# Kernel tuning notes

Measured on AMD Instinct MI355X. Metric: run time of the kernel, lower is better.

## Reference

```python
import jax, jax.numpy as jnp
import numpy as np

K_REGION = 32
C_CONTEXT = 128
CONF_THR = 0.5


def safe_normalize(x):
    return x / jnp.maximum(x.sum(axis=-1, keepdims=True), 1e-6)


def _geometry(mask_grid, h, w):
    # mask_grid: [B, K, h*w] -> per-mask bbox (x_min,y_min,x_max,y_max) + area, vectorized
    B, K, _ = mask_grid.shape
    m2 = mask_grid.reshape(B, K, h, w)
    present = m2 > 0.05
    rows = present.any(-1)  # [B,K,h]
    cols = present.any(-2)  # [B,K,w]
    yi = jnp.arange(h)
    xi = jnp.arange(w)
    y_min = jnp.min(jnp.where(rows, yi, h), axis=-1).astype(jnp.float32)
    y_max = jnp.max(jnp.where(rows, yi, -1), axis=-1).astype(jnp.float32)
    x_min = jnp.min(jnp.where(cols, xi, w), axis=-1).astype(jnp.float32)
    x_max = jnp.max(jnp.where(cols, xi, -1), axis=-1).astype(jnp.float32)
    hden = float(max(h - 1, 1))
    wden = float(max(w - 1, 1))
    area = present.astype(jnp.float32).mean(axis=(-1, -2))
    geom = jnp.stack([x_min / wden, y_min / hden, x_max / wden, y_max / hden, area], axis=-1)
    has_any = present.any(axis=(-1, -2))
    return jnp.where(has_any[..., None], geom, 0.0).astype(mask_grid.dtype)


def setup_inputs():
    key = jax.random.key(0)
    ks = jax.random.split(key, 16)
    B, N, D, M, Hm, Wm, Qd, Hd = 8, 576, 1024, 64, 384, 384, 4096, 1024
    inp = {}
    inp['patch_tokens'] = jax.random.normal(ks[0], (B, N, D), jnp.float32)
    inp['masks'] = jax.random.uniform(ks[1], (B, M, Hm, Wm), jnp.float32)
    inp['scores'] = jax.random.uniform(ks[2], (B, M), jnp.float32)
    inp['question_embed'] = jax.random.normal(ks[3], (B, Qd), jnp.float32)
    s = 0.02
    inp['W1'] = jax.random.normal(ks[4], (5, D), jnp.float32) * s
    inp['b1'] = jnp.zeros((D,), jnp.float32)
    inp['W2'] = jax.random.normal(ks[5], (D, D), jnp.float32) * s
    inp['b2'] = jnp.zeros((D,), jnp.float32)
    inp['Wv'] = jax.random.normal(ks[6], (D, Hd), jnp.float32) * s
    inp['bv'] = jnp.zeros((Hd,), jnp.float32)
    inp['Wp'] = jax.random.normal(ks[7], (1, Hd), jnp.float32) * s
    inp['bp'] = jnp.zeros((Hd,), jnp.float32)
    inp['Wq'] = jax.random.normal(ks[8], (Qd, Hd), jnp.float32) * s
    inp['bq'] = jnp.zeros((Hd,), jnp.float32)
    inp['Wo'] = jax.random.normal(ks[9], (Hd, 1), jnp.float32) * s
    inp['bo'] = jnp.zeros((1,), jnp.float32)
    inp['type_emb'] = jax.random.normal(ks[10], (3, D), jnp.float32) * s
    inp['patch_h'] = 24
    inp['patch_w'] = 24
    return inp


def reference(patch_tokens, masks, scores, question_embed, W1, b1, W2, b2,
              Wv, bv, Wp, bp, Wq, bq, Wo, bo, type_emb, patch_h, patch_w):
    B, N, D = patch_tokens.shape
    h, w = patch_h, patch_w
    M = masks.shape[1]

    grounding_valid = (masks.reshape(B, M, -1).sum(-1) > 0).any(-1)  # [B]

    order = jnp.argsort(-scores, axis=1)
    scores_s = jnp.take_along_axis(scores, order, axis=1)
    masks_s = jnp.take_along_axis(masks, order[:, :, None, None], axis=1)
    masks_k = masks_s[:, :K_REGION]
    scores_k = scores_s[:, :K_REGION]
    valid = scores_k >= CONF_THR
    masks_k = masks_k * valid[:, :, None, None].astype(masks_k.dtype)
    scores_k = jnp.where(valid, scores_k, 0.0)

    # MaskDownsampler: adaptive avg pool (exact: Hm,Wm divisible by h,w)
    Hm, Wm = masks_k.shape[-2:]
    fh, fw = Hm // h, Wm // w
    mg = masks_k.reshape(B, K_REGION, h, fh, w, fw).mean(axis=(3, 5)).reshape(B, K_REGION, h * w)

    uniform = jnp.full((B, K_REGION, N), 1.0 / N, dtype=patch_tokens.dtype)
    mg = jnp.where(grounding_valid[:, None, None], mg, uniform)
    scores_k = jnp.where(grounding_valid[:, None], scores_k, 1.0)

    # RegionPooler
    nm = safe_normalize(jnp.maximum(mg, 0.0))
    pooled = jnp.einsum('bkn,bnd->bkd', nm, patch_tokens)
    weighted = pooled * scores_k[..., None]
    geom = _geometry(mg, h, w)  # [B,K,5]
    g = jax.nn.silu(geom @ W1 + b1) @ W2 + b2
    region_tokens = weighted + g

    patch_prior = (mg * scores_k[..., None]).sum(axis=1)
    patch_prior = safe_normalize(jnp.maximum(patch_prior, 0.0))
    patch_prior = jnp.where(grounding_valid[:, None], patch_prior, jnp.full_like(patch_prior, 1.0 / N))

    # RoutingScorer
    hid = jnp.tanh(patch_tokens @ Wv + bv
                   + patch_prior[:, :, None] @ Wp + bp
                   + (question_embed @ Wq + bq)[:, None, :])
    routing_scores = (hid @ Wo + bo)[..., 0]  # [B,N]
    routing_weights = jax.nn.softmax(routing_scores, axis=-1)

    top_k = min(C_CONTEXT, N)
    _, sel_idx = jax.lax.top_k(routing_scores, top_k)
    context_tokens = jnp.take_along_axis(patch_tokens, sel_idx[:, :, None], axis=1)
    sel_mask = jnp.zeros((B, N), patch_tokens.dtype).at[jnp.arange(B)[:, None], sel_idx].set(1.0)

    # BackgroundPooler
    residual = jnp.maximum(1.0 - sel_mask, 0.0)
    residual = residual / jnp.maximum(residual.sum(-1, keepdims=True), 1e-6)
    bg = jnp.einsum('bn,bnd->bd', residual, patch_tokens)

    region_tokens = region_tokens + type_emb[0][None, None, :]
    context_tokens = context_tokens + type_emb[1][None, None, :]
    background_token = bg[:, None, :] + type_emb[2][None, None, :]
    visual_tokens = jnp.concatenate([region_tokens, context_tokens, background_token], axis=1)

    return (visual_tokens, region_tokens, context_tokens, background_token,
            patch_prior, routing_weights, sel_idx, grounding_valid)
```

## Files before the change

### kernel.cpp

```cpp
#include <hip/hip_runtime.h>
#include <math.h>

typedef long long I64;

#define NB    8
#define NTOK  576
#define DIM   1024
#define NMASK 64
#define HMASK 384
#define WMASK 384
#define QDIM  4096
#define HDIM  1024
#define KREG  32
#define CCTX  128
#define GH    24
#define GW    24
#define GNUM  576

#define OFF_VIS 0
#define OFF_REG 1318912
#define OFF_CTX 1581056
#define OFF_BG  2629632
#define OFF_PP  2637824
#define OFF_RW  2642432
#define OFF_SEL 2647040
#define OFF_GV  2648064

#define WS_BS   0
#define WS_NMAT 294912
#define WS_SCK  442368
#define WS_H1   442624
#define WS_Q    704768
#define WS_Q2   712960
#define WS_GV   721152
#define WS_PP   721160
#define WS_CS   725768
#define WS_RS   733960
#define WS_RSP  738568
#define WS_HID  775432
#define WS_END  5494024

#define QBLK      256
#define BS_BLOCKS (NB * NMASK * 24)
#define MEGA_GRID (256 + 256 + BS_BLOCKS)

__global__ __launch_bounds__(256, 2) void k_mega(
    const float* __restrict__ masks, const float* __restrict__ qe,
    const float* __restrict__ Wq, const float* __restrict__ bq,
    const float* __restrict__ pt, const float* __restrict__ Wv,
    float* __restrict__ ws) {
  int gid = blockIdx.x;
  int t = threadIdx.x;
  __shared__ __align__(16) float smem[10432];

  if (gid < 256) {
    int b = gid >> 5;
    int r = gid & 31;
    int tokTile = r >> 3;
    int colTile = r & 7;
    int n0 = tokTile * 144;
    int col0 = colTile * 128;
    int trow = t >> 4;
    int tcol = t & 15;

    float (*sA)[36]  = (float(*)[36])smem;
    float (*sW)[164] = (float(*)[164])(smem + 5184);

    float acc[9][8];
    #pragma unroll
    for (int i = 0; i < 9; ++i)
      #pragma unroll
      for (int j = 0; j < 8; ++j) acc[i][j] = 0.f;

    int a_row0 = t >> 3, a_kq = t & 7;
    int a_row1 = (t + 256) >> 3;
    int a_row2 = (t + 512) >> 3;
    int a_row3 = (t + 768) >> 3;
    int a_row4 = (t + 1024) >> 3;
    int w_k0 = t >> 5, w_c = t & 31;

    const float* ptb = pt + (I64)(b * NTOK + n0) * DIM;
    const float* wvb = Wv + col0;

    float4 pa0, pa1, pa2, pa3, pa4 = {0,0,0,0};
    float4 pw0, pw1, pw2, pw3;

    pa0 = *(const float4*)&ptb[(I64)a_row0 * DIM + a_kq * 4];
    pa1 = *(const float4*)&ptb[(I64)a_row1 * DIM + a_kq * 4];
    pa2 = *(const float4*)&ptb[(I64)a_row2 * DIM + a_kq * 4];
    pa3 = *(const float4*)&ptb[(I64)a_row3 * DIM + a_kq * 4];
    if (t < 128) pa4 = *(const float4*)&ptb[(I64)a_row4 * DIM + a_kq * 4];
    pw0 = *(const float4*)&wvb[(I64)(w_k0 +  0) * HDIM + w_c * 4];
    pw1 = *(const float4*)&wvb[(I64)(w_k0 +  8) * HDIM + w_c * 4];
    pw2 = *(const float4*)&wvb[(I64)(w_k0 + 16) * HDIM + w_c * 4];
    pw3 = *(const float4*)&wvb[(I64)(w_k0 + 24) * HDIM + w_c * 4];

    for (int s = 0; s < 32; ++s) {
      __syncthreads();
      *(float4*)&sA[a_row0][a_kq * 4] = pa0;
      *(float4*)&sA[a_row1][a_kq * 4] = pa1;
      *(float4*)&sA[a_row2][a_kq * 4] = pa2;
      *(float4*)&sA[a_row3][a_kq * 4] = pa3;
      if (t < 128) *(float4*)&sA[a_row4][a_kq * 4] = pa4;
      *(float4*)&sW[w_k0 +  0][w_c * 4] = pw0;
      *(float4*)&sW[w_k0 +  8][w_c * 4] = pw1;
      *(float4*)&sW[w_k0 + 16][w_c * 4] = pw2;
      *(float4*)&sW[w_k0 + 24][w_c * 4] = pw3;
      __syncthreads();
      if (s + 1 < 32) {
        int k0 = (s + 1) * 32;
        pa0 = *(const float4*)&ptb[(I64)a_row0 * DIM + k0 + a_kq * 4];
        pa1 = *(const float4*)&ptb[(I64)a_row1 * DIM + k0 + a_kq * 4];
        pa2 = *(const float4*)&ptb[(I64)a_row2 * DIM + k0 + a_kq * 4];
        pa3 = *(const float4*)&ptb[(I64)a_row3 * DIM + k0 + a_kq * 4];
        if (t < 128) pa4 = *(const float4*)&ptb[(I64)a_row4 * DIM + k0 + a_kq * 4];
        pw0 = *(const float4*)&wvb[(I64)(k0 + w_k0 +  0) * HDIM + w_c * 4];
        pw1 = *(const float4*)&wvb[(I64)(k0 + w_k0 +  8) * HDIM + w_c * 4];
        pw2 = *(const float4*)&wvb[(I64)(k0 + w_k0 + 16) * HDIM + w_c * 4];
        pw3 = *(const float4*)&wvb[(I64)(k0 + w_k0 + 24) * HDIM + w_c * 4];
      }
      #pragma unroll 2
      for (int kk4 = 0; kk4 < 8; ++kk4) {
        float4 af[9];
        #pragma unroll
        for (int i = 0; i < 9; ++i)
          af[i] = *(const float4*)&sA[trow * 9 + i][kk4 * 4];
        float4 w0[4], w1[4];
        #pragma unroll
        for (int m = 0; m < 4; ++m) {
          w0[m] = *(const float4*)&sW[kk4 * 4 + m][tcol * 4];
          w1[m] = *(const float4*)&sW[kk4 * 4 + m][64 + tcol * 4];
        }
        #pragma unroll
        for (int i = 0; i < 9; ++i) {
          #pragma unroll
          for (int m = 0; m < 4; ++m) {
            float a = ((const float*)&af[i])[m];
            acc[i][0] = fmaf(a, w0[m].x, acc[i][0]);
            acc[i][1] = fmaf(a, w0[m].y, acc[i][1]);
            acc[i][2] = fmaf(a, w0[m].z, acc[i][2]);
            acc[i][3] = fmaf(a, w0[m].w, acc[i][3]);
            acc[i][4] = fmaf(a, w1[m].x, acc[i][4]);
            acc[i][5] = fmaf(a, w1[m].y, acc[i][5]);
            acc[i][6] = fmaf(a, w1[m].z, acc[i][6]);
            acc[i][7] = fmaf(a, w1[m].w, acc[i][7]);
          }
        }
      }
    }
    float* hid = ws + WS_HID + ((I64)b * NTOK + n0) * HDIM;
    #pragma unroll
    for (int i = 0; i < 9; ++i) {
      int row = trow * 9 + i;
      float4 va = {acc[i][0], acc[i][1], acc[i][2], acc[i][3]};
      float4 vb = {acc[i][4], acc[i][5], acc[i][6], acc[i][7]};
      *(float4*)&hid[(I64)row * HDIM + col0 + tcol * 4] = va;
      *(float4*)&hid[(I64)row * HDIM + col0 + 64 + tcol * 4] = vb;
    }
  } else if (gid < 512) {
    int g = gid - 256;
    int b = g >> 5, r = g & 31;
    int qb = r >> 1, ih = r & 1;
    int base = ih * 2048;
    float* qs = smem;
    float (*sp)[64] = (float(*)[64])(smem + 2048);
    const float4* s4 = (const float4*)(qe + (I64)b * QDIM + base);
    *(float4*)&qs[t * 4] = s4[t];
    *(float4*)&qs[(t + 256) * 4] = s4[t + 256];
    __syncthreads();
    int dl = t & 63, ig = t >> 6;
    int d = qb * 64 + dl;
    const float* wq = Wq + d;
    float a0 = 0.f, a1 = 0.f, a2 = 0.f, a3 = 0.f;
    float a4 = 0.f, a5 = 0.f, a6 = 0.f, a7 = 0.f;
    for (int i = ig; i < 2048; i += 32) {
      a0 = fmaf(qs[i],      wq[(I64)(base + i) * HDIM],      a0);
      a1 = fmaf(qs[i + 4],  wq[(I64)(base + i + 4) * HDIM],  a1);
      a2 = fmaf(qs[i + 8],  wq[(I64)(base + i + 8) * HDIM],  a2);
      a3 = fmaf(qs[i + 12], wq[(I64)(base + i + 12) * HDIM], a3);
      a4 = fmaf(qs[i + 16], wq[(I64)(base + i + 16) * HDIM], a4);
      a5 = fmaf(qs[i + 20], wq[(I64)(base + i + 20) * HDIM], a5);
      a6 = fmaf(qs[i + 24], wq[(I64)(base + i + 24) * HDIM], a6);
      a7 = fmaf(qs[i + 28], wq[(I64)(base + i + 28) * HDIM], a7);
    }
    sp[ig][dl] = ((a0 + a1) + (a2 + a3)) + ((a4 + a5) + (a6 + a7));
    __syncthreads();
    if (t < 64) {
      float s2 = (sp[0][t] + sp[1][t]) + (sp[2][t] + sp[3][t]);
      int dd = qb * 64 + t;
      ws[(ih ? WS_Q2 : WS_Q) + (I64)b * HDIM + dd] = s2 + (ih ? 0.f : bq[dd]);
    }
  } else {
    int g = gid - 512;
    int yband = g % 24;
    int bm = g / 24;
    float (*sm)[96] = (float(*)[96])smem;
    const float4* src = (const float4*)(masks + (I64)bm * (HMASK * WMASK) + (I64)yband * 16 * WMASK);
    #pragma unroll
    for (int j = 0; j < 6; ++j) {
      int f = t + 256 * j;
      float4 v = src[f];
      sm[f / 96][f % 96] = (v.x + v.y) + (v.z + v.w);
    }
    __syncthreads();
    if (t < 24) {
      float tt = 0.f;
      #pragma unroll
      for (int rr = 0; rr < 16; ++rr)
        #pragma unroll
        for (int c = 0; c < 4; ++c) tt += sm[rr][t * 4 + c];
      ws[WS_BS + (I64)bm * GNUM + yband * 24 + t] = tt;
    }
  }
}

__global__ __launch_bounds__(256) void k_epi(
    const float* __restrict__ bv, const float* __restrict__ bp,
    const float* __restrict__ Wp, const float* __restrict__ Wo,
    const float* __restrict__ bo, float* __restrict__ ws) {
  int t = threadIdx.x;
  int g = blockIdx.x * 16 + (t >> 4);
  int l = t & 15;
  int b = g / NTOK, n = g % NTOK;
  const float* hid = ws + WS_HID + (I64)g * HDIM;
  const float* q1 = ws + WS_Q + (I64)b * HDIM;
  const float* q2 = ws + WS_Q2 + (I64)b * HDIM;
  float ppv = ws[WS_PP + b * GNUM + n];
  float ssum = 0.f;
  #pragma unroll 4
  for (int j = 0; j < 16; ++j) {
    int c = l * 64 + j * 4;
    float4 h4 = *(const float4*)&hid[c];
    float4 b4 = *(const float4*)&bv[c];
    float4 p4 = *(const float4*)&bp[c];
    float4 w4 = *(const float4*)&Wp[c];
    float4 o4 = *(const float4*)&Wo[c];
    float4 qa = *(const float4*)&q1[c];
    float4 qb = *(const float4*)&q2[c];
    ssum = fmaf(o4.x, tanhf(h4.x + b4.x + p4.x + qa.x + qb.x + ppv * w4.x), ssum);
    ssum = fmaf(o4.y, tanhf(h4.y + b4.y + p4.y + qa.y + qb.y + ppv * w4.y), ssum);
    ssum = fmaf(o4.z, tanhf(h4.z + b4.z + p4.z + qa.z + qb.z + ppv * w4.z), ssum);
    ssum = fmaf(o4.w, tanhf(h4.w + b4.w + p4.w + qa.w + qb.w + ppv * w4.w), ssum);
  }
  ssum += __shfl_xor(ssum, 1);
  ssum += __shfl_xor(ssum, 2);
  ssum += __shfl_xor(ssum, 4);
  ssum += __shfl_xor(ssum, 8);
  if (l == 0) ws[WS_RS + g] = ssum + bo[0];
}

#define MGPAD 580
__global__ __launch_bounds__(256) void k_perbatch(
    const float* __restrict__ bs, const float* __restrict__ scores,
    const float* __restrict__ W1, const float* __restrict__ b1,
    float* __restrict__ ws, float* __restrict__ out) {
  int b = blockIdx.x;
  int t = threadIdx.x;
  __shared__ float s_mg[KREG][MGPAD];
  __shared__ float s_sc[NMASK];
  __shared__ float s_msum[NMASK];
  __shared__ int   s_order[NMASK];
  __shared__ float s_sck[KREG];
  __shared__ int   s_valid[KREG];
  __shared__ int   s_midx[KREG];
  __shared__ float s_rowsum[KREG];
  __shared__ float s_pp[GNUM];
  __shared__ float s_geom[KREG][5];
  __shared__ float s_red[64];
  __shared__ int   s_gv;
  __shared__ float s_ppsum;

  {
    int m = t >> 2, q = t & 3;
    const float4* p = (const float4*)(bs + ((I64)b * NMASK + m) * GNUM) + q * 36;
    float s = 0.f;
    #pragma unroll 4
    for (int j = 0; j < 36; ++j) {
      float4 v = p[j];
      s += v.x; s += v.y; s += v.z; s += v.w;
    }
    s += __shfl_xor(s, 1);
    s += __shfl_xor(s, 2);
    if (q == 0) s_msum[m] = s;
  }
  if (t < NMASK) s_sc[t] = scores[b * NMASK + t];
  __syncthreads();
  if (t == 0) {
    int g = 0;
    for (int m = 0; m < NMASK; ++m) g |= (s_msum[m] > 0.f) ? 1 : 0;
    s_gv = g;
  }
  if (t < NMASK) {
    float v = s_sc[t];
    int r = 0;
    for (int j = 0; j < NMASK; ++j) {
      float vj = s_sc[j];
      r += (vj > v) || (vj == v && j < t);
    }
    s_order[r] = t;
  }
  __syncthreads();
  const int gv = s_gv;
  if (t < KREG) {
    int m = s_order[t];
    float sc = s_sc[m];
    int valid = (sc >= 0.5f) ? 1 : 0;
    s_midx[t] = m;
    s_valid[t] = valid;
    float sck = gv ? (valid ? sc : 0.f) : 1.f;
    s_sck[t] = sck;
    ws[WS_SCK + b * KREG + t] = sck;
  }
  __syncthreads();
  {
    int k = t >> 3, sub = t & 7;
    const float inv256 = 1.f / 256.f;
    const float invN = 1.f / 576.f;
    float scale = gv ? (s_valid[k] ? inv256 : 0.f) : 0.f;
    float addv  = gv ? 0.f : invN;
    const float4* src = (const float4*)(bs + ((I64)b * NMASK + s_midx[k]) * GNUM) + sub * 18;
    float* dst = &s_mg[k][sub * 72];
    #pragma unroll 3
    for (int j = 0; j < 18; ++j) {
      float4 v = src[j];
      v.x = v.x * scale + addv;
      v.y = v.y * scale + addv;
      v.z = v.z * scale + addv;
      v.w = v.w * scale + addv;
      *(float4*)(dst + j * 4) = v;
    }
  }
// ... 14 lines not shown
    ws[WS_NMAT + ((I64)b * KREG + k) * GNUM + n] = v / fmaxf(s_rowsum[k], 1e-6f);
  }
  for (int n = t; n < GNUM; n += 256) {
    float raw = 0.f;
    #pragma unroll
    for (int k = 0; k < KREG; ++k) raw = fmaf(s_mg[k][n], s_sck[k], raw);
    s_pp[n] = fmaxf(raw, 0.f);
  }
  __syncthreads();
  if (t < 64) {
    float s = 0.f;
    for (int n = t; n < GNUM; n += 64) s += s_pp[n];
    s_red[t] = s;
  }
  __syncthreads();
  if (t == 0) {
    float s = 0.f;
    for (int i = 0; i < 64; ++i) s += s_red[i];
    s_ppsum = s;
  }
  __syncthreads();
  {
    const float invN = 1.f / 576.f;
    float den = fmaxf(s_ppsum, 1e-6f);
    for (int n = t; n < GNUM; n += 256) {
      float v = gv ? (s_pp[n] / den) : invN;
      ws[WS_PP + b * GNUM + n] = v;
      out[OFF_PP + b * GNUM + n] = v;
    }
  }
  {
    int k = t >> 3, sub = t & 7;
    unsigned colmask = 0u;
    int ymin = GH, ymax = -1, cnt = 0;
    #pragma unroll
    for (int yy = 0; yy < 3; ++yy) {
      int y = sub * 3 + yy;
      unsigned rowm = 0u;
      for (int x = 0; x < GW; ++x)
        if (s_mg[k][y * GW + x] > 0.05f) rowm |= (1u << x);
      if (rowm) { if (y < ymin) ymin = y; if (y > ymax) ymax = y; }
      colmask |= rowm;
      cnt += __popc(rowm);
    }
    #pragma unroll
    for (int off = 1; off < 8; off <<= 1) {
      colmask |= (unsigned)__shfl_xor((int)colmask, off);
      cnt += __shfl_xor(cnt, off);
      int o1 = __shfl_xor(ymin, off); ymin = (o1 < ymin) ? o1 : ymin;
      int o2 = __shfl_xor(ymax, off); ymax = (o2 > ymax) ? o2 : ymax;
    }
    if (sub == 0) {
      float g0, g1, g2, g3, g4;
      if (cnt > 0) {
        int xmin = __ffs(colmask) - 1;
        int xmax = 31 - __clz(colmask);
        g0 = (float)xmin / 23.f;
        g1 = (float)ymin / 23.f;
        g2 = (float)xmax / 23.f;
        g3 = (float)ymax / 23.f;
        g4 = (float)cnt / 576.f;
      } else { g0 = g1 = g2 = g3 = g4 = 0.f; }
      s_geom[k][0] = g0; s_geom[k][1] = g1; s_geom[k][2] = g2;
      s_geom[k][3] = g3; s_geom[k][4] = g4;
    }
  }
  __syncthreads();
  for (int idx = t; idx < KREG * HDIM; idx += 256) {
    int k = idx >> 10, j = idx & 1023;
    float x = 0.f;
    #pragma unroll
    for (int i = 0; i < 5; ++i) x += s_geom[k][i] * W1[i * HDIM + j];
    x += b1[j];
    float sg = 1.f / (1.f + expf(-x));
    ws[WS_H1 + ((I64)b * KREG + k) * HDIM + j] = x * sg;
  }
  if (t == 0) {
    float g = gv ? 1.f : 0.f;
    ws[WS_GV + b] = g;
    out[OFF_GV + b] = g;
  }
}

__global__ __launch_bounds__(512) void k_region(
    const float* __restrict__ pt, const float* __restrict__ W2,
    const float* __restrict__ b2, const float* __restrict__ te,
    float* __restrict__ ws, float* __restrict__ out) {
  int blk = blockIdx.x;
  int b = blk >> 6, kg = (blk >> 3) & 7, dg = blk & 7;
  int t = threadIdx.x;
  int dl = t & 127;
  int qh = t >> 7;
  int d = dg * 128 + dl;
  const float* nmb = ws + WS_NMAT + ((I64)b * KREG + kg * 4) * GNUM;
  const float* h1b = ws + WS_H1 + ((I64)b * KREG + kg * 4) * HDIM;
  float accP[4] = {0, 0, 0, 0};
  float accG[4] = {0, 0, 0, 0};
  float accS = 0.f;
  int n0 = qh * 144, n1 = n0 + 144;
  for (int n = n0; n < n1; ++n) {
    float p = pt[((I64)b * NTOK + n) * DIM + d];
    accS += p;
    #pragma unroll
    for (int kk = 0; kk < 4; ++kk)
      accP[kk] = fmaf(nmb[kk * GNUM + n], p, accP[kk]);
  }
  int j0 = qh * 256, j1 = j0 + 256;
  for (int j = j0; j < j1; ++j) {
    float wv = W2[(I64)j * DIM + d];
    #pragma unroll
    for (int kk = 0; kk < 4; ++kk)
      accG[kk] = fmaf(h1b[kk * HDIM + j], wv, accG[kk]);
  }
  __shared__ float cmbP[4][4][128];
  __shared__ float cmbG[4][4][128];
  __shared__ float cmbS[4][128];
  #pragma unroll
  for (int kk = 0; kk < 4; ++kk) {
    cmbP[qh][kk][dl] = accP[kk];
    cmbG[qh][kk][dl] = accG[kk];
  }
  cmbS[qh][dl] = accS;
  __syncthreads();
  if (qh == 0) {
    float bb = b2[d], t0 = te[d];
    #pragma unroll
    for (int kk = 0; kk < 4; ++kk) {
      int k = kg * 4 + kk;
      float P = (cmbP[0][kk][dl] + cmbP[1][kk][dl]) + (cmbP[2][kk][dl] + cmbP[3][kk][dl]);
      float G = (cmbG[0][kk][dl] + cmbG[1][kk][dl]) + (cmbG[2][kk][dl] + cmbG[3][kk][dl]);
      float val = P * ws[WS_SCK + b * KREG + k] + G + bb + t0;
      out[OFF_REG + ((I64)b * KREG + k) * DIM + d] = val;
      out[OFF_VIS + ((I64)b * 161 + k) * DIM + d] = val;
    }
    if (kg == 0)
      ws[WS_CS + (I64)b * DIM + d] =
          (cmbS[0][dl] + cmbS[1][dl]) + (cmbS[2][dl] + cmbS[3][dl]);
  }
}

__global__ __launch_bounds__(576) void k_soft2(float* __restrict__ ws, float* __restrict__ out) {
  int b = blockIdx.x, t = threadIdx.x;
  __shared__ float s_rs[NTOK];
  __shared__ float s_w[9];
  __shared__ float s_max, s_sum;
  s_rs[t] = ws[WS_RS + b * NTOK + t];
  __syncthreads();
  float v = s_rs[t];
  int r = 0;
  for (int j = 0; j < NTOK; ++j) {
    float vj = s_rs[j];
    r += (vj > v) || (vj == v && j < t);
  }
  float m = v;
  for (int off = 1; off < 64; off <<= 1) m = fmaxf(m, __shfl_xor(m, off));
  if ((t & 63) == 0) s_w[t >> 6] = m;
  __syncthreads();
  if (t == 0) {
    float mm = s_w[0];
    for (int i = 1; i < 9; ++i) mm = fmaxf(mm, s_w[i]);
    s_max = mm;
  }
  __syncthreads();
  float e = expf(v - s_max);
  float s = e;
  for (int off = 1; off < 64; off <<= 1) s += __shfl_xor(s, off);
  if ((t & 63) == 0) s_w[t >> 6] = s;
  __syncthreads();
  if (t == 0) {
    float ss = 0.f;
    for (int i = 0; i < 9; ++i) ss += s_w[i];
    s_sum = ss;
  }
  __syncthreads();
  out[OFF_RW + b * NTOK + t] = e / s_sum;
  if (r < CCTX) out[OFF_SEL + b * CCTX + r] = (float)t;
}

__global__ __launch_bounds__(256) void k_post(const float* __restrict__ pt, const float* __restrict__ te,
                                              const float* __restrict__ ws, const float* __restrict__ outr,
                                              float* __restrict__ out) {
  int rr = blockIdx.x, b = blockIdx.y;
  int d = threadIdx.x * 4;
  if (rr < CCTX) {
    int idx = (int)outr[OFF_SEL + b * CCTX + rr];
    float4 v = *(const float4*)&pt[((I64)b * NTOK + idx) * DIM + d];
    float4 e = *(const float4*)&te[DIM + d];
    v.x += e.x; v.y += e.y; v.z += e.z; v.w += e.w;
    *(float4*)&out[OFF_CTX + ((I64)b * CCTX + rr) * DIM + d] = v;
    *(float4*)&out[OFF_VIS + ((I64)b * 161 + KREG + rr) * DIM + d] = v;
  } else {
    float4 s = *(const float4*)&ws[WS_CS + (I64)b * DIM + d];
    for (int r = 0; r < CCTX; ++r) {
      int idx = (int)outr[OFF_SEL + b * CCTX + r];
      float4 v = *(const float4*)&pt[((I64)b * NTOK + idx) * DIM + d];
      s.x -= v.x; s.y -= v.y; s.z -= v.z; s.w -= v.w;
    }
    const float rinv = 1.f / 448.f;
    float4 e = *(const float4*)&te[2 * DIM + d];
    float4 o;
    o.x = s.x * rinv + e.x; o.y = s.y * rinv + e.y;
    o.z = s.z * rinv + e.z; o.w = s.w * rinv + e.w;
    *(float4*)&out[OFF_BG + (I64)b * DIM + d] = o;
    *(float4*)&out[OFF_VIS + ((I64)b * 161 + 160) * DIM + d] = o;
  }
}

__global__ __launch_bounds__(384) void k_bsq(const float* __restrict__ masks,
                                             const float* __restrict__ qe,
                                             const float* __restrict__ Wq,
                                             const float* __restrict__ bq,
                                             float* __restrict__ ws) {
  int gid = blockIdx.x;
  int t = threadIdx.x;
  __shared__ float shm[2048 + 6 * 64];
  if (gid >= QBLK) {
    int gid2 = gid - QBLK;
    int yband = gid2 % 24;
    int bm = gid2 / 24;
    float (*sm)[96] = (float(*)[96])shm;
    const float4* src = (const float4*)(masks + (I64)bm * (HMASK * WMASK) + (I64)yband * 16 * WMASK);
    float4 s4 = src[t];
    float4 v1 = src[t + 384];
    float4 v2 = src[t + 768];
    float4 v3 = src[t + 1152];
    s4.x += v1.x; s4.y += v1.y; s4.z += v1.z; s4.w += v1.w;
    s4.x += v2.x; s4.y += v2.y; s4.z += v2.z; s4.w += v2.w;
    s4.x += v3.x; s4.y += v3.y; s4.z += v3.z; s4.w += v3.w;
    float s = (s4.x + s4.y) + (s4.z + s4.w);
    sm[t / 96][t % 96] = s;
    __syncthreads();
    if (t < 24) {
      float tt = 0.f;
      #pragma unroll
      for (int rg = 0; rg < 4; ++rg)
        #pragma unroll
        for (int c = 0; c < 4; ++c) tt += sm[rg][t * 4 + c];
      ws[WS_BS + (I64)bm * GNUM + yband * 24 + t] = tt;
    }
  } else {
    int b = gid >> 5;
    int r = gid & 31;
    int qb = r >> 1;
    int ih = r & 1;
    int base = ih * 2048;
    float* qs = shm;
    float (*sp)[64] = (float(*)[64])(shm + 2048);
    {
      const float4* s4 = (const float4*)(qe + (I64)b * QDIM + base);
      float4 v = s4[t];
      *(float4*)&qs[t * 4] = v;
      if (t < 128) {
        float4 v2 = s4[t + 384];
        *(float4*)&qs[(t + 384) * 4] = v2;
      }
    }
    __syncthreads();
    int dl = t & 63, ig = t >> 6;
    int d = qb * 64 + dl;
    const float* wq = Wq + d;
    float a0 = 0.f, a1 = 0.f, a2 = 0.f, a3 = 0.f;
    float a4 = 0.f, a5 = 0.f, a6 = 0.f, a7 = 0.f;
    int i = ig;
    for (; i + 42 < 2048; i += 48) {
      a0 = fmaf(qs[i],      wq[(I64)(base + i) * HDIM],      a0);
      a1 = fmaf(qs[i + 6],  wq[(I64)(base + i + 6) * HDIM],  a1);
      a2 = fmaf(qs[i + 12], wq[(I64)(base + i + 12) * HDIM], a2);
      a3 = fmaf(qs[i + 18], wq[(I64)(base + i + 18) * HDIM], a3);
      a4 = fmaf(qs[i + 24], wq[(I64)(base + i + 24) * HDIM], a4);
      a5 = fmaf(qs[i + 30], wq[(I64)(base + i + 30) * HDIM], a5);
      a6 = fmaf(qs[i + 36], wq[(I64)(base + i + 36) * HDIM], a6);
      a7 = fmaf(qs[i + 42], wq[(I64)(base + i + 42) * HDIM], a7);
    }
    for (; i < 2048; i += 6)
      a0 = fmaf(qs[i], wq[(I64)(base + i) * HDIM], a0);
    sp[ig][dl] = ((a0 + a1) + (a2 + a3)) + ((a4 + a5) + (a6 + a7));
    __syncthreads();
    if (t < 64) {
      float s2 = ((sp[0][t] + sp[1][t]) + (sp[2][t] + sp[3][t])) + (sp[4][t] + sp[5][t]);
      int dd = qb * 64 + t;
      float outv = s2 + (ih ? 0.f : bq[dd]);
      ws[(ih ? WS_Q2 : WS_Q) + (I64)b * HDIM + dd] = outv;
    }
  }
}

__global__ __launch_bounds__(256, 1) void k_hid4(
// ... 76 lines not shown
      #pragma unroll
      for (int i = 0; i < 9; ++i)
        af[i] = *(const float4*)&sA[cur][trow * 9 + i][kk4 * 4];
      float4 w0[4], w1[4];
      #pragma unroll
      for (int m = 0; m < 4; ++m) {
        w0[m] = *(const float4*)&sW[cur][kk4 * 4 + m][tcol * 4];
        w1[m] = *(const float4*)&sW[cur][kk4 * 4 + m][64 + tcol * 4];
      }
      #pragma unroll
      for (int i = 0; i < 9; ++i) {
        #pragma unroll
        for (int m = 0; m < 4; ++m) {
          float a = ((const float*)&af[i])[m];
          acc[i][0] = fmaf(a, w0[m].x, acc[i][0]);
          acc[i][1] = fmaf(a, w0[m].y, acc[i][1]);
          acc[i][2] = fmaf(a, w0[m].z, acc[i][2]);
          acc[i][3] = fmaf(a, w0[m].w, acc[i][3]);
          acc[i][4] = fmaf(a, w1[m].x, acc[i][4]);
          acc[i][5] = fmaf(a, w1[m].y, acc[i][5]);
          acc[i][6] = fmaf(a, w1[m].z, acc[i][6]);
          acc[i][7] = fmaf(a, w1[m].w, acc[i][7]);
        }
      }
    }
    if (s + 1 < 32) {
      int nxt = (s + 1) & 1;
      *(float4*)&sA[nxt][a_row0][a_kq0 * 4] = pa0;
      *(float4*)&sA[nxt][a_row1][a_kq0 * 4] = pa1;
      *(float4*)&sA[nxt][a_row2][a_kq0 * 4] = pa2;
      *(float4*)&sA[nxt][a_row3][a_kq0 * 4] = pa3;
      if (t < 128) *(float4*)&sA[nxt][a_row4][a_kq0 * 4] = pa4;
      *(float4*)&sW[nxt][w_k0 +  0][w_c * 4] = pw0;
      *(float4*)&sW[nxt][w_k0 +  8][w_c * 4] = pw1;
      *(float4*)&sW[nxt][w_k0 + 16][w_c * 4] = pw2;
      *(float4*)&sW[nxt][w_k0 + 24][w_c * 4] = pw3;
    }
  }

  int ca = col0 + tcol * 4;
  int cb = col0 + 64 + tcol * 4;
  float4 bvA = *(const float4*)&bv[ca], bvB = *(const float4*)&bv[cb];
  float4 bpA = *(const float4*)&bp[ca], bpB = *(const float4*)&bp[cb];
  float4 wpA = *(const float4*)&Wp[ca], wpB = *(const float4*)&Wp[cb];
  float4 woA = *(const float4*)&Wo[ca], woB = *(const float4*)&Wo[cb];
  float4 qaA = *(const float4*)&ws[WS_Q  + (I64)b * HDIM + ca];
  float4 qaB = *(const float4*)&ws[WS_Q  + (I64)b * HDIM + cb];
  float4 qbA = *(const float4*)&ws[WS_Q2 + (I64)b * HDIM + ca];
  float4 qbB = *(const float4*)&ws[WS_Q2 + (I64)b * HDIM + cb];
  float bvv[8] = {bvA.x, bvA.y, bvA.z, bvA.w, bvB.x, bvB.y, bvB.z, bvB.w};
  float bpv[8] = {bpA.x, bpA.y, bpA.z, bpA.w, bpB.x, bpB.y, bpB.z, bpB.w};
  float wpv[8] = {wpA.x, wpA.y, wpA.z, wpA.w, wpB.x, wpB.y, wpB.z, wpB.w};
  float wov[8] = {woA.x, woA.y, woA.z, woA.w, woB.x, woB.y, woB.z, woB.w};
  float qv[8]  = {qaA.x + qbA.x, qaA.y + qbA.y, qaA.z + qbA.z, qaA.w + qbA.w,
                  qaB.x + qbB.x, qaB.y + qbB.y, qaB.z + qbB.z, qaB.w + qbB.w};
  float partial[9];
  #pragma unroll
  for (int i = 0; i < 9; ++i) {
    float ppv = ws[WS_PP + b * GNUM + n0 + trow * 9 + i];
    float s = 0.f;
    #pragma unroll
    for (int j = 0; j < 8; ++j) {
      float pre = acc[i][j] + bvv[j] + bpv[j] + qv[j] + ppv * wpv[j];
      s = fmaf(wov[j], tanhf(pre), s);
    }
    partial[i] = s;
  }
  #pragma unroll
  for (int i = 0; i < 9; ++i) {
    float p = partial[i];
    p += __shfl_xor(p, 1);
    p += __shfl_xor(p, 2);
    p += __shfl_xor(p, 4);
    p += __shfl_xor(p, 8);
    partial[i] = p;
  }
  if (tcol == 0) {
    #pragma unroll
    for (int i = 0; i < 9; ++i)
      ws[WS_RSP + ((I64)b * NTOK + n0 + trow * 9 + i) * 8 + colTile] = partial[i];
  }
}

__global__ __launch_bounds__(576) void k_soft_fb(const float* __restrict__ bo,
                                                 float* __restrict__ ws, float* __restrict__ out) {
  int b = blockIdx.x, t = threadIdx.x;
  __shared__ float s_rs[NTOK];
  __shared__ float s_w[9];
  __shared__ float s_max, s_sum;
  {
    const float4* p = (const float4*)(ws + WS_RSP + ((I64)b * NTOK + t) * 8);
    float4 v0 = p[0], v1 = p[1];
    s_rs[t] = bo[0] + (((v0.x + v0.y) + (v0.z + v0.w)) + ((v1.x + v1.y) + (v1.z + v1.w)));
  }
  __syncthreads();
  float v = s_rs[t];
  int r = 0;
  for (int j = 0; j < NTOK; ++j) {
    float vj = s_rs[j];
    r += (vj > v) || (vj == v && j < t);
  }
  float m = v;
  for (int off = 1; off < 64; off <<= 1) m = fmaxf(m, __shfl_xor(m, off));
  if ((t & 63) == 0) s_w[t >> 6] = m;
  __syncthreads();
  if (t == 0) {
    float mm = s_w[0];
    for (int i = 1; i < 9; ++i) mm = fmaxf(mm, s_w[i]);
    s_max = mm;
  }
  __syncthreads();
  float e = expf(v - s_max);
  float s = e;
  for (int off = 1; off < 64; off <<= 1) s += __shfl_xor(s, off);
  if ((t & 63) == 0) s_w[t >> 6] = s;
  __syncthreads();
  if (t == 0) {
    float ss = 0.f;
    for (int i = 0; i < 9; ++i) ss += s_w[i];
    s_sum = ss;
  }
  __syncthreads();
  out[OFF_RW + b * NTOK + t] = e / s_sum;
  if (r < CCTX) out[OFF_SEL + b * CCTX + r] = (float)t;
}

extern "C" void kernel_launch(void* const* d_in, const int* in_sizes, int n_in,
                              void* d_out, int out_size, void* d_ws, size_t ws_size,
                              hipStream_t stream) {
  (void)in_sizes; (void)n_in; (void)out_size;
  const float* pt     = (const float*)d_in[0];
  const float* masks  = (const float*)d_in[1];
  const float* scores = (const float*)d_in[2];
  const float* qe     = (const float*)d_in[3];
  const float* W1     = (const float*)d_in[4];
  const float* b1     = (const float*)d_in[5];
  const float* W2     = (const float*)d_in[6];
  const float* b2     = (const float*)d_in[7];
  const float* Wv     = (const float*)d_in[8];
  const float* bv     = (const float*)d_in[9];
  const float* Wp     = (const float*)d_in[10];
  const float* bp     = (const float*)d_in[11];
  const float* Wq     = (const float*)d_in[12];
  const float* bq     = (const float*)d_in[13];
  const float* Wo     = (const float*)d_in[14];
  const float* bo     = (const float*)d_in[15];
  const float* te     = (const float*)d_in[16];
  float* out = (float*)d_out;
  float* ws  = (float*)d_ws;

  if (ws_size >= (size_t)WS_END * 4) {
    k_mega<<<dim3(MEGA_GRID), dim3(256), 0, stream>>>(masks, qe, Wq, bq, pt, Wv, ws);
    k_perbatch<<<dim3(NB), dim3(256), 0, stream>>>(ws + WS_BS, scores, W1, b1, ws, out);
    k_epi<<<dim3(288), dim3(256), 0, stream>>>(bv, bp, Wp, Wo, bo, ws);
    k_region<<<dim3(512), dim3(512), 0, stream>>>(pt, W2, b2, te, ws, out);
    k_soft2<<<dim3(NB), dim3(576), 0, stream>>>(ws, out);
    k_post<<<dim3(CCTX + 1, NB), dim3(256), 0, stream>>>(pt, te, ws, out, out);
  } else {
    k_bsq<<<dim3(QBLK + BS_BLOCKS), dim3(384), 0, stream>>>(masks, qe, Wq, bq, ws);
    k_perbatch<<<dim3(NB), dim3(256), 0, stream>>>(ws + WS_BS, scores, W1, b1, ws, out);
    k_region<<<dim3(512), dim3(512), 0, stream>>>(pt, W2, b2, te, ws, out);
    k_hid4<<<dim3(256), dim3(256), 0, stream>>>(pt, Wv, bv, Wp, bp, Wo, ws);
    k_soft_fb<<<dim3(NB), dim3(576), 0, stream>>>(bo, ws, out);
    k_post<<<dim3(CCTX + 1, NB), dim3(256), 0, stream>>>(pt, te, ws, out, out);
  }
}
```

Baseline: 328.0 us.

## Enlarge hid GEMM tiles, fuse routing epilogue into region kernel, parallelize bg pooling

```diff
diff --git a/kernel.cpp b/kernel.cpp
--- a/kernel.cpp
+++ b/kernel.cpp
@@ -42,7 +42,8 @@
 
 #define QBLK      256
 #define BS_BLOCKS (NB * NMASK * 24)
-#define MEGA_GRID (256 + 256 + BS_BLOCKS)
+#define HIDBLK    192
+#define MEGA_GRID (HIDBLK + 256 + BS_BLOCKS)
 
 __global__ __launch_bounds__(256, 2) void k_mega(
     const float* __restrict__ masks, const float* __restrict__ qe,
@@ -51,45 +52,39 @@
     float* __restrict__ ws) {
   int gid = blockIdx.x;
   int t = threadIdx.x;
-  __shared__ __align__(16) float smem[10432];
-
-  if (gid < 256) {
-    int b = gid >> 5;
-    int r = gid & 31;
+  __shared__ __align__(16) float smem[12160];
+
+  if (gid < HIDBLK) {
+    int b = gid / 24;
+    int r = gid % 24;
     int tokTile = r >> 3;
     int colTile = r & 7;
-    int n0 = tokTile * 144;
+    int n0 = tokTile * 192;
     int col0 = colTile * 128;
     int trow = t >> 4;
     int tcol = t & 15;
 
     float (*sA)[36]  = (float(*)[36])smem;
-    float (*sW)[164] = (float(*)[164])(smem + 5184);
-
-    float acc[9][8];
-    #pragma unroll
-    for (int i = 0; i < 9; ++i)
+    float (*sW)[164] = (float(*)[164])(smem + 6912);
+
+    float acc[12][8];
+    #pragma unroll
+    for (int i = 0; i < 12; ++i)
       #pragma unroll
       for (int j = 0; j < 8; ++j) acc[i][j] = 0.f;
 
-    int a_row0 = t >> 3, a_kq = t & 7;
-    int a_row1 = (t + 256) >> 3;
-    int a_row2 = (t + 512) >> 3;
-    int a_row3 = (t + 768) >> 3;
-    int a_row4 = (t + 1024) >> 3;
+    int a_row = t >> 3, a_kq = t & 7;
     int w_k0 = t >> 5, w_c = t & 31;
 
     const float* ptb = pt + (I64)(b * NTOK + n0) * DIM;
     const float* wvb = Wv + col0;
 
-    float4 pa0, pa1, pa2, pa3, pa4 = {0,0,0,0};
+    float4 pa[6];
     float4 pw0, pw1, pw2, pw3;
 
-    pa0 = *(const float4*)&ptb[(I64)a_row0 * DIM + a_kq * 4];
-    pa1 = *(const float4*)&ptb[(I64)a_row1 * DIM + a_kq * 4];
-    pa2 = *(const float4*)&ptb[(I64)a_row2 * DIM + a_kq * 4];
-    pa3 = *(const float4*)&ptb[(I64)a_row3 * DIM + a_kq * 4];
-    if (t < 128) pa4 = *(const float4*)&ptb[(I64)a_row4 * DIM + a_kq * 4];
+    #pragma unroll
+    for (int j = 0; j < 6; ++j)
+      pa[j] = *(const float4*)&ptb[(I64)(a_row + 32 * j) * DIM + a_kq * 4];
     pw0 = *(const float4*)&wvb[(I64)(w_k0 +  0) * HDIM + w_c * 4];
     pw1 = *(const float4*)&wvb[(I64)(w_k0 +  8) * HDIM + w_c * 4];
     pw2 = *(const float4*)&wvb[(I64)(w_k0 + 16) * HDIM + w_c * 4];
@@ -97,11 +92,9 @@
 
     for (int s = 0; s < 32; ++s) {
       __syncthreads();
-      *(float4*)&sA[a_row0][a_kq * 4] = pa0;
-      *(float4*)&sA[a_row1][a_kq * 4] = pa1;
-      *(float4*)&sA[a_row2][a_kq * 4] = pa2;
-      *(float4*)&sA[a_row3][a_kq * 4] = pa3;
-      if (t < 128) *(float4*)&sA[a_row4][a_kq * 4] = pa4;
+      #pragma unroll
+      for (int j = 0; j < 6; ++j)
+        *(float4*)&sA[a_row + 32 * j][a_kq * 4] = pa[j];
       *(float4*)&sW[w_k0 +  0][w_c * 4] = pw0;
       *(float4*)&sW[w_k0 +  8][w_c * 4] = pw1;
       *(float4*)&sW[w_k0 + 16][w_c * 4] = pw2;
@@ -109,11 +102,9 @@
       __syncthreads();
       if (s + 1 < 32) {
         int k0 = (s + 1) * 32;
-        pa0 = *(const float4*)&ptb[(I64)a_row0 * DIM + k0 + a_kq * 4];
-        pa1 = *(const float4*)&ptb[(I64)a_row1 * DIM + k0 + a_kq * 4];
-        pa2 = *(const float4*)&ptb[(I64)a_row2 * DIM + k0 + a_kq * 4];
-        pa3 = *(const float4*)&ptb[(I64)a_row3 * DIM + k0 + a_kq * 4];
-        if (t < 128) pa4 = *(const float4*)&ptb[(I64)a_row4 * DIM + k0 + a_kq * 4];
+        #pragma unroll
+        for (int j = 0; j < 6; ++j)
+          pa[j] = *(const float4*)&ptb[(I64)(a_row + 32 * j) * DIM + k0 + a_kq * 4];
         pw0 = *(const float4*)&wvb[(I64)(k0 + w_k0 +  0) * HDIM + w_c * 4];
         pw1 = *(const float4*)&wvb[(I64)(k0 + w_k0 +  8) * HDIM + w_c * 4];
         pw2 = *(const float4*)&wvb[(I64)(k0 + w_k0 + 16) * HDIM + w_c * 4];
@@ -121,44 +112,67 @@
       }
       #pragma unroll 2
       for (int kk4 = 0; kk4 < 8; ++kk4) {
-        float4 af[9];
-        #pragma unroll
-        for (int i = 0; i < 9; ++i)
-          af[i] = *(const float4*)&sA[trow * 9 + i][kk4 * 4];
         float4 w0[4], w1[4];
         #pragma unroll
         for (int m = 0; m < 4; ++m) {
           w0[m] = *(const float4*)&sW[kk4 * 4 + m][tcol * 4];
           w1[m] = *(const float4*)&sW[kk4 * 4 + m][64 + tcol * 4];
         }
-        #pragma unroll
-        for (int i = 0; i < 9; ++i) {
+        {
+          float4 af[6];
           #pragma unroll
-          for (int m = 0; m < 4; ++m) {
-            float a = ((const float*)&af[i])[m];
-            acc[i][0] = fmaf(a, w0[m].x, acc[i][0]);
-            acc[i][1] = fmaf(a, w0[m].y, acc[i][1]);
-            acc[i][2] = fmaf(a, w0[m].z, acc[i][2]);
-            acc[i][3] = fmaf(a, w0[m].w, acc[i][3]);
-            acc[i][4] = fmaf(a, w1[m].x, acc[i][4]);
-            acc[i][5] = fmaf(a, w1[m].y, acc[i][5]);
-            acc[i][6] = fmaf(a, w1[m].z, acc[i][6]);
-            acc[i][7] = fmaf(a, w1[m].w, acc[i][7]);
+          for (int i = 0; i < 6; ++i)
+            af[i] = *(const float4*)&sA[trow * 12 + i][kk4 * 4];
+          #pragma unroll
+          for (int i = 0; i < 6; ++i) {
+            #pragma unroll
+            for (int m = 0; m < 4; ++m) {
+              float a = ((const float*)&af[i])[m];
+              acc[i][0] = fmaf(a, w0[m].x, acc[i][0]);
+              acc[i][1] = fmaf(a, w0[m].y, acc[i][1]);
+              acc[i][2] = fmaf(a, w0[m].z, acc[i][2]);
+              acc[i][3] = fmaf(a, w0[m].w, acc[i][3]);
+              acc[i][4] = fmaf(a, w1[m].x, acc[i][4]);
+              acc[i][5] = fmaf(a, w1[m].y, acc[i][5]);
+              acc[i][6] = fmaf(a, w1[m].z, acc[i][6]);
+              acc[i][7] = fmaf(a, w1[m].w, acc[i][7]);
+            }
+          }
+        }
+        {
+          float4 af[6];
+          #pragma unroll
+          for (int i = 0; i < 6; ++i)
+            af[i] = *(const float4*)&sA[trow * 12 + 6 + i][kk4 * 4];
+          #pragma unroll
+          for (int i = 0; i < 6; ++i) {
+            #pragma unroll
+            for (int m = 0; m < 4; ++m) {
+              float a = ((const float*)&af[i])[m];
+              acc[6 + i][0] = fmaf(a, w0[m].x, acc[6 + i][0]);
+              acc[6 + i][1] = fmaf(a, w0[m].y, acc[6 + i][1]);
+              acc[6 + i][2] = fmaf(a, w0[m].z, acc[6 + i][2]);
+              acc[6 + i][3] = fmaf(a, w0[m].w, acc[6 + i][3]);
+              acc[6 + i][4] = fmaf(a, w1[m].x, acc[6 + i][4]);
+              acc[6 + i][5] = fmaf(a, w1[m].y, acc[6 + i][5]);
+              acc[6 + i][6] = fmaf(a, w1[m].z, acc[6 + i][6]);
+              acc[6 + i][7] = fmaf(a, w1[m].w, acc[6 + i][7]);
+            }
           }
         }
       }
     }
     float* hid = ws + WS_HID + ((I64)b * NTOK + n0) * HDIM;
     #pragma unroll
-    for (int i = 0; i < 9; ++i) {
-      int row = trow * 9 + i;
+    for (int i = 0; i < 12; ++i) {
+      int row = trow * 12 + i;
       float4 va = {acc[i][0], acc[i][1], acc[i][2], acc[i][3]};
       float4 vb = {acc[i][4], acc[i][5], acc[i][6], acc[i][7]};
       *(float4*)&hid[(I64)row * HDIM + col0 + tcol * 4] = va;
       *(float4*)&hid[(I64)row * HDIM + col0 + 64 + tcol * 4] = vb;
     }
-  } else if (gid < 512) {
-    int g = gid - 256;
+  } else if (gid < HIDBLK + 256) {
+    int g = gid - HIDBLK;
     int b = g >> 5, r = g & 31;
     int qb = r >> 1, ih = r & 1;
     int base = ih * 2048;
@@ -191,7 +205,7 @@
       ws[(ih ? WS_Q2 : WS_Q) + (I64)b * HDIM + dd] = s2 + (ih ? 0.f : bq[dd]);
     }
   } else {
-    int g = gid - 512;
+    int g = gid - (HIDBLK + 256);
     int yband = g % 24;
     int bm = g / 24;
     float (*sm)[96] = (float(*)[96])smem;
@@ -212,41 +226,6 @@
       ws[WS_BS + (I64)bm * GNUM + yband * 24 + t] = tt;
     }
   }
-}
-
-__global__ __launch_bounds__(256) void k_epi(
-    const float* __restrict__ bv, const float* __restrict__ bp,
-    const float* __restrict__ Wp, const float* __restrict__ Wo,
-    const float* __restrict__ bo, float* __restrict__ ws) {
-  int t = threadIdx.x;
-  int g = blockIdx.x * 16 + (t >> 4);
-  int l = t & 15;
-  int b = g / NTOK, n = g % NTOK;
-  const float* hid = ws + WS_HID + (I64)g * HDIM;
-  const float* q1 = ws + WS_Q + (I64)b * HDIM;
-  const float* q2 = ws + WS_Q2 + (I64)b * HDIM;
-  float ppv = ws[WS_PP + b * GNUM + n];
-  float ssum = 0.f;
-  #pragma unroll 4
-  for (int j = 0; j < 16; ++j) {
-    int c = l * 64 + j * 4;
-    float4 h4 = *(const float4*)&hid[c];
-    float4 b4 = *(const float4*)&bv[c];
-    float4 p4 = *(const float4*)&bp[c];
-    float4 w4 = *(const float4*)&Wp[c];
-    float4 o4 = *(const float4*)&Wo[c];
-    float4 qa = *(const float4*)&q1[c];
-    float4 qb = *(const float4*)&q2[c];
-    ssum = fmaf(o4.x, tanhf(h4.x + b4.x + p4.x + qa.x + qb.x + ppv * w4.x), ssum);
-    ssum = fmaf(o4.y, tanhf(h4.y + b4.y + p4.y + qa.y + qb.y + ppv * w4.y), ssum);
-    ssum = fmaf(o4.z, tanhf(h4.z + b4.z + p4.z + qa.z + qb.z + ppv * w4.z), ssum);
-    ssum = fmaf(o4.w, tanhf(h4.w + b4.w + p4.w + qa.w + qb.w + ppv * w4.w), ssum);
-  }
-  ssum += __shfl_xor(ssum, 1);
-  ssum += __shfl_xor(ssum, 2);
-  ssum += __shfl_xor(ssum, 4);
-  ssum += __shfl_xor(ssum, 8);
-  if (l == 0) ws[WS_RS + g] = ssum + bo[0];
 }
 
 #define MGPAD 580
@@ -427,60 +406,94 @@
   }
 }
 
-__global__ __launch_bounds__(512) void k_region(
+__global__ __launch_bounds__(512) void k_regepi(
     const float* __restrict__ pt, const float* __restrict__ W2,
     const float* __restrict__ b2, const float* __restrict__ te,
+    const float* __restrict__ bv, const float* __restrict__ bp,
+    const float* __restrict__ Wp, const float* __restrict__ Wo,
+    const float* __restrict__ bo,
     float* __restrict__ ws, float* __restrict__ out) {
   int blk = blockIdx.x;
-  int b = blk >> 6, kg = (blk >> 3) & 7, dg = blk & 7;
   int t = threadIdx.x;
-  int dl = t & 127;
-  int qh = t >> 7;
-  int d = dg * 128 + dl;
-  const float* nmb = ws + WS_NMAT + ((I64)b * KREG + kg * 4) * GNUM;
-  const float* h1b = ws + WS_H1 + ((I64)b * KREG + kg * 4) * HDIM;
-  float accP[4] = {0, 0, 0, 0};
-  float accG[4] = {0, 0, 0, 0};
-  float accS = 0.f;
-  int n0 = qh * 144, n1 = n0 + 144;
-  for (int n = n0; n < n1; ++n) {
-    float p = pt[((I64)b * NTOK + n) * DIM + d];
-    accS += p;
-    #pragma unroll
-    for (int kk = 0; kk < 4; ++kk)
-      accP[kk] = fmaf(nmb[kk * GNUM + n], p, accP[kk]);
-  }
-  int j0 = qh * 256, j1 = j0 + 256;
-  for (int j = j0; j < j1; ++j) {
-    float wv = W2[(I64)j * DIM + d];
-    #pragma unroll
-    for (int kk = 0; kk < 4; ++kk)
-      accG[kk] = fmaf(h1b[kk * HDIM + j], wv, accG[kk]);
-  }
-  __shared__ float cmbP[4][4][128];
-  __shared__ float cmbG[4][4][128];
-  __shared__ float cmbS[4][128];
-  #pragma unroll
-  for (int kk = 0; kk < 4; ++kk) {
-    cmbP[qh][kk][dl] = accP[kk];
-    cmbG[qh][kk][dl] = accG[kk];
-  }
-  cmbS[qh][dl] = accS;
-  __syncthreads();
-  if (qh == 0) {
-    float bb = b2[d], t0 = te[d];
+  if (blk < 512) {
+    int b = blk >> 6, kg = (blk >> 3) & 7, dg = blk & 7;
+    int dl = t & 127;
+    int qh = t >> 7;
+    int d = dg * 128 + dl;
+    const float* nmb = ws + WS_NMAT + ((I64)b * KREG + kg * 4) * GNUM;
+    const float* h1b = ws + WS_H1 + ((I64)b * KREG + kg * 4) * HDIM;
+    float accP[4] = {0, 0, 0, 0};
+    float accG[4] = {0, 0, 0, 0};
+    float accS = 0.f;
+    int n0 = qh * 144, n1 = n0 + 144;
+    for (int n = n0; n < n1; ++n) {
+      float p = pt[((I64)b * NTOK + n) * DIM + d];
+      accS += p;
+      #pragma unroll
+      for (int kk = 0; kk < 4; ++kk)
+        accP[kk] = fmaf(nmb[kk * GNUM + n], p, accP[kk]);
+    }
+    int j0 = qh * 256, j1 = j0 + 256;
+    for (int j = j0; j < j1; ++j) {
+      float wv = W2[(I64)j * DIM + d];
+      #pragma unroll
+      for (int kk = 0; kk < 4; ++kk)
+        accG[kk] = fmaf(h1b[kk * HDIM + j], wv, accG[kk]);
+    }
+    __shared__ float cmbP[4][4][128];
+    __shared__ float cmbG[4][4][128];
+    __shared__ float cmbS[4][128];
     #pragma unroll
     for (int kk = 0; kk < 4; ++kk) {
-      int k = kg * 4 + kk;
-      float P = (cmbP[0][kk][dl] + cmbP[1][kk][dl]) + (cmbP[2][kk][dl] + cmbP[3][kk][dl]);
-      float G = (cmbG[0][kk][dl] + cmbG[1][kk][dl]) + (cmbG[2][kk][dl] + cmbG[3][kk][dl]);
-      float val = P * ws[WS_SCK + b * KREG + k] + G + bb + t0;
-      out[OFF_REG + ((I64)b * KREG + k) * DIM + d] = val;
-      out[OFF_VIS + ((I64)b * 161 + k) * DIM + d] = val;
-    }
-    if (kg == 0)
-      ws[WS_CS + (I64)b * DIM + d] =
-          (cmbS[0][dl] + cmbS[1][dl]) + (cmbS[2][dl] + cmbS[3][dl]);
+      cmbP[qh][kk][dl] = accP[kk];
+      cmbG[qh][kk][dl] = accG[kk];
+    }
+    cmbS[qh][dl] = accS;
+    __syncthreads();
+    if (qh == 0) {
+      float bb = b2[d], t0 = te[d];
+      #pragma unroll
+      for (int kk = 0; kk < 4; ++kk) {
+        int k = kg * 4 + kk;
+        float P = (cmbP[0][kk][dl] + cmbP[1][kk][dl]) + (cmbP[2][kk][dl] + cmbP[3][kk][dl]);
+        float G = (cmbG[0][kk][dl] + cmbG[1][kk][dl]) + (cmbG[2][kk][dl] + cmbG[3][kk][dl]);
+        float val = P * ws[WS_SCK + b * KREG + k] + G + bb + t0;
+        out[OFF_REG + ((I64)b * KREG + k) * DIM + d] = val;
+        out[OFF_VIS + ((I64)b * 161 + k) * DIM + d] = val;
+      }
+      if (kg == 0)
+        ws[WS_CS + (I64)b * DIM + d] =
+            (cmbS[0][dl] + cmbS[1][dl]) + (cmbS[2][dl] + cmbS[3][dl]);
+    }
+  } else {
+    int g = (blk - 512) * 32 + (t >> 4);
+    int l = t & 15;
+    int b = g / NTOK, n = g % NTOK;
+    const float* hid = ws + WS_HID + (I64)g * HDIM;
+    const float* q1 = ws + WS_Q + (I64)b * HDIM;
+    const float* q2 = ws + WS_Q2 + (I64)b * HDIM;
+    float ppv = ws[WS_PP + b * GNUM + n];
+    float ssum = 0.f;
+    #pragma unroll 4
+    for (int j = 0; j < 16; ++j) {
+      int c = l * 64 + j * 4;
+      float4 h4 = *(const float4*)&hid[c];
+      float4 b4 = *(const float4*)&bv[c];
+      float4 p4 = *(const float4*)&bp[c];
+      float4 w4 = *(const float4*)&Wp[c];
+      float4 o4 = *(const float4*)&Wo[c];
+      float4 qa = *(const float4*)&q1[c];
+      float4 qb = *(const float4*)&q2[c];
+      ssum = fmaf(o4.x, tanhf(h4.x + b4.x + p4.x + qa.x + qb.x + ppv * w4.x), ssum);
+      ssum = fmaf(o4.y, tanhf(h4.y + b4.y + p4.y + qa.y + qb.y + ppv * w4.y), ssum);
+      ssum = fmaf(o4.z, tanhf(h4.z + b4.z + p4.z + qa.z + qb.z + ppv * w4.z), ssum);
+      ssum = fmaf(o4.w, tanhf(h4.w + b4.w + p4.w + qa.w + qb.w + ppv * w4.w), ssum);
+    }
+    ssum += __shfl_xor(ssum, 1);
+    ssum += __shfl_xor(ssum, 2);
+    ssum += __shfl_xor(ssum, 4);
+    ssum += __shfl_xor(ssum, 8);
+    if (l == 0) ws[WS_RS + g] = ssum + bo[0];
   }
 }
 
@@ -526,8 +539,8 @@
                                               const float* __restrict__ ws, const float* __restrict__ outr,
                                               float* __restrict__ out) {
   int rr = blockIdx.x, b = blockIdx.y;
-  int d = threadIdx.x * 4;
   if (rr < CCTX) {
+    int d = threadIdx.x * 4;
     int idx = (int)outr[OFF_SEL + b * CCTX + rr];
     float4 v = *(const float4*)&pt[((I64)b * NTOK + idx) * DIM + d];
     float4 e = *(const float4*)&te[DIM + d];
@@ -535,19 +548,35 @@
     *(float4*)&out[OFF_CTX + ((I64)b * CCTX + rr) * DIM + d] = v;
     *(float4*)&out[OFF_VIS + ((I64)b * 161 + KREG + rr) * DIM + d] = v;
   } else {
-    float4 s = *(const float4*)&ws[WS_CS + (I64)b * DIM + d];
-    for (int r = 0; r < CCTX; ++r) {
-      int idx = (int)outr[OFF_SEL + b * CCTX + r];
-      float4 v = *(const float4*)&pt[((I64)b * NTOK + idx) * DIM + d];
-      s.x -= v.x; s.y -= v.y; s.z -= v.z; s.w -= v.w;
-    }
-    const float rinv = 1.f / 448.f;
-    float4 e = *(const float4*)&te[2 * DIM + d];
-    float4 o;
-    o.x = s.x * rinv + e.x; o.y = s.y * rinv + e.y;
-    o.z = s.z * rinv + e.z; o.w = s.w * rinv + e.w;
-    *(float4*)&out[OFF_BG + (I64)b * DIM + d] = o;
-    *(float4*)&out[OFF_VIS + ((I64)b * 161 + 160) * DIM + d] = o;
+    int dl = threadIdx.x & 63;
+    int rg = threadIdx.x >> 6;
+    __shared__ float4 cmb[4][64];
+    #pragma unroll
+    for (int dd = 0; dd < 4; ++dd) {
+      int d = (dd * 64 + dl) * 4;
+      float4 s = {0.f, 0.f, 0.f, 0.f};
+      for (int r = rg * 32; r < rg * 32 + 32; ++r) {
+        int idx = (int)outr[OFF_SEL + b * CCTX + r];
+        float4 v = *(const float4*)&pt[((I64)b * NTOK + idx) * DIM + d];
+        s.x += v.x; s.y += v.y; s.z += v.z; s.w += v.w;
+      }
+      cmb[rg][dl] = s;
+      __syncthreads();
+      if (rg == 0) {
+        float4 s0 = cmb[0][dl], s1 = cmb[1][dl], s2 = cmb[2][dl], s3 = cmb[3][dl];
+        float4 cs = *(const float4*)&ws[WS_CS + (I64)b * DIM + d];
+        const float rinv = 1.f / 448.f;
+        float4 e = *(const float4*)&te[2 * DIM + d];
+        float4 o;
+        o.x = (cs.x - ((s0.x + s1.x) + (s2.x + s3.x))) * rinv + e.x;
+        o.y = (cs.y - ((s0.y + s1.y) + (s2.y + s3.y))) * rinv + e.y;
+        o.z = (cs.z - ((s0.z + s1.z) + (s2.z + s3.z))) * rinv + e.z;
+        o.w = (cs.w - ((s0.w + s1.w) + (s2.w + s3.w))) * rinv + e.w;
+        *(float4*)&out[OFF_BG + (I64)b * DIM + d] = o;
+        *(float4*)&out[OFF_VIS + ((I64)b * 161 + 160) * DIM + d] = o;
+      }
+      __syncthreads();
+    }
   }
 }
 
@@ -790,6 +819,63 @@
   }
 }
 
+__global__ __launch_bounds__(512) void k_region_fb(
+    const float* __restrict__ pt, const float* __restrict__ W2,
+    const float* __restrict__ b2, const float* __restrict__ te,
+    float* __restrict__ ws, float* __restrict__ out) {
+  int blk = blockIdx.x;
+  int b = blk >> 6, kg = (blk >> 3) & 7, dg = blk & 7;
+  int t = threadIdx.x;
+  int dl = t & 127;
+  int qh = t >> 7;
+  int d = dg * 128 + dl;
+  const float* nmb = ws + WS_NMAT + ((I64)b * KREG + kg * 4) * GNUM;
+  const float* h1b = ws + WS_H1 + ((I64)b * KREG + kg * 4) * HDIM;
+  float accP[4] = {0, 0, 0, 0};
+  float accG[4] = {0, 0, 0, 0};
+  float accS = 0.f;
+  int n0 = qh * 144, n1 = n0 + 144;
+  for (int n = n0; n < n1; ++n) {
+    float p = pt[((I64)b * NTOK + n) * DIM + d];
+    accS += p;
+    #pragma unroll
+    for (int kk = 0; kk < 4; ++kk)
+      accP[kk] = fmaf(nmb[kk * GNUM + n], p, accP[kk]);
+  }
+  int j0 = qh * 256, j1 = j0 + 256;
+  for (int j = j0; j < j1; ++j) {
+    float wv = W2[(I64)j * DIM + d];
+    #pragma unroll
+    for (int kk = 0; kk < 4; ++kk)
+      accG[kk] = fmaf(h1b[kk * HDIM + j], wv, accG[kk]);
+  }
+  __shared__ float cmbP[4][4][128];
+  __shared__ float cmbG[4][4][128];
+  __shared__ float cmbS[4][128];
+  #pragma unroll
+  for (int kk = 0; kk < 4; ++kk) {
+    cmbP[qh][kk][dl] = accP[kk];
+    cmbG[qh][kk][dl] = accG[kk];
+  }
+  cmbS[qh][dl] = accS;
+  __syncthreads();
+  if (qh == 0) {
+    float bb = b2[d], t0 = te[d];
+    #pragma unroll
+    for (int kk = 0; kk < 4; ++kk) {
+      int k = kg * 4 + kk;
+      float P = (cmbP[0][kk][dl] + cmbP[1][kk][dl]) + (cmbP[2][kk][dl] + cmbP[3][kk][dl]);
+      float G = (cmbG[0][kk][dl] + cmbG[1][kk][dl]) + (cmbG[2][kk][dl] + cmbG[3][kk][dl]);
+      float val = P * ws[WS_SCK + b * KREG + k] + G + bb + t0;
+      out[OFF_REG + ((I64)b * KREG + k) * DIM + d] = val;
+      out[OFF_VIS + ((I64)b * 161 + k) * DIM + d] = val;
+    }
+    if (kg == 0)
+      ws[WS_CS + (I64)b * DIM + d] =
+          (cmbS[0][dl] + cmbS[1][dl]) + (cmbS[2][dl] + cmbS[3][dl]);
+  }
+}
+
 __global__ __launch_bounds__(576) void k_soft_fb(const float* __restrict__ bo,
                                                  float* __restrict__ ws, float* __restrict__ out) {
   int b = blockIdx.x, t = threadIdx.x;
@@ -860,14 +946,13 @@
   if (ws_size >= (size_t)WS_END * 4) {
     k_mega<<<dim3(MEGA_GRID), dim3(256), 0, stream>>>(masks, qe, Wq, bq, pt, Wv, ws);
     k_perbatch<<<dim3(NB), dim3(256), 0, stream>>>(ws + WS_BS, scores, W1, b1, ws, out);
-    k_epi<<<dim3(288), dim3(256), 0, stream>>>(bv, bp, Wp, Wo, bo, ws);
-    k_region<<<dim3(512), dim3(512), 0, stream>>>(pt, W2, b2, te, ws, out);
+    k_regepi<<<dim3(512 + 144), dim3(512), 0, stream>>>(pt, W2, b2, te, bv, bp, Wp, Wo, bo, ws, out);
     k_soft2<<<dim3(NB), dim3(576), 0, stream>>>(ws, out);
     k_post<<<dim3(CCTX + 1, NB), dim3(256), 0, stream>>>(pt, te, ws, out, out);
   } else {
     k_bsq<<<dim3(QBLK + BS_BLOCKS), dim3(384), 0, stream>>>(masks, qe, Wq, bq, ws);
     k_perbatch<<<dim3(NB), dim3(256), 0, stream>>>(ws + WS_BS, scores, W1, b1, ws, out);
-    k_region<<<dim3(512), dim3(512), 0, stream>>>(pt, W2, b2, te, ws, out);
+    k_region_fb<<<dim3(512), dim3(512), 0, stream>>>(pt, W2, b2, te, ws, out);
     k_hid4<<<dim3(256), dim3(256), 0, stream>>>(pt, Wv, bv, Wp, bp, Wo, ws);
     k_soft_fb<<<dim3(NB), dim3(576), 0, stream>>>(bo, ws, out);
     k_post<<<dim3(CCTX + 1, NB), dim3(256), 0, stream>>>(pt, te, ws, out, out);
```

Result: slower. 381.6 us (+16.4%).
